# Kernel tuning notes

Measured on AMD Instinct MI355X. Metric: run time of the kernel, lower is better.

The kernel has to match this reference:

```python
import jax, jax.numpy as jnp
import numpy as np

N_SA_ITERS = 3
MESH_LR = 5.0
MESH_ITERS = 4
SH_ITERS = 5
EPS = 1e-8
B, N, D, S, H = 16, 16384, 64, 7, 128


def layer_norm(x, g, b):
    m = jnp.mean(x, -1, keepdims=True)
    v = jnp.var(x, -1, keepdims=True)
    return (x - m) * jax.lax.rsqrt(v + 1e-5) * g + b


def cdist(k, q):
    # k: [b,n,d], q: [b,s,d] -> euclidean distances [b,n,s]
    k2 = jnp.sum(k * k, -1)[:, :, None]
    q2 = jnp.sum(q * q, -1)[:, None, :]
    sq = k2 + q2 - 2.0 * jnp.einsum('bnd,bsd->bns', k, q)
    return jnp.sqrt(jnp.maximum(sq, 0.0) + 1e-12)


def sinkhorn(C, log_a, log_b, u, v, n_iters=SH_ITERS):
    # log-domain Sinkhorn. C: [b,n,s], log_a: [b,n], log_b: [b,s]
    p = -C
    for _ in range(n_iters):
        u = log_a - jax.nn.logsumexp(p + v[:, None, :], axis=2)
        v = log_b - jax.nn.logsumexp(p + u[:, :, None], axis=1)
    T = jnp.exp(p + u[:, :, None] + v[:, None, :])
    return T, u, v


def minimize_entropy_of_sinkhorn(C, log_a, log_b, mesh_lr=MESH_LR, n_mesh_iters=MESH_ITERS):
    # MESH: gradient descent on transport-plan entropy wrt the cost matrix,
    # warm-starting the sinkhorn duals across mesh iterations.
    u = jnp.zeros_like(log_a)
    v = jnp.zeros_like(log_b)
    for _ in range(n_mesh_iters):
        def ent(Cc, uu, vv):
            T, u2, v2 = sinkhorn(Cc, log_a, log_b, uu, vv)
            e = -jnp.sum(T * jnp.log(T + EPS))
            return e, (u2, v2)
        (_, (u, v)), g = jax.value_and_grad(ent, has_aux=True)(
            C, jax.lax.stop_gradient(u), jax.lax.stop_gradient(v))
        C = C - mesh_lr * g
    return C, u, v


def gru_cell(x, h, W_ih, W_hh, b_ih, b_hh):
    # PyTorch nn.GRUCell semantics
    gi = x @ W_ih.T + b_ih
    gh = h @ W_hh.T + b_hh
    i_r, i_z, i_n = jnp.split(gi, 3, axis=-1)
    h_r, h_z, h_n = jnp.split(gh, 3, axis=-1)
    r = jax.nn.sigmoid(i_r + h_r)
    z = jax.nn.sigmoid(i_z + h_z)
    n = jnp.tanh(i_n + r * h_n)
    return (1.0 - z) * n + z * h


def setup_inputs() -> dict:
    key = jax.random.key(0)
    ks = jax.random.split(key, 24)
    w = lambda k, shape, s=0.05: (jax.random.normal(k, shape, dtype=jnp.float32) * s)
    return {
        'inputs': jax.random.normal(ks[0], (B, N, D), dtype=jnp.float32),
        'slots_init': jax.random.normal(ks[1], (B, S, D), dtype=jnp.float32),
        'slots_mu': w(ks[2], (1, 1, D), 0.1),
        'slots_log_sigma': w(ks[3], (1, 1, D), 0.1),
        'Wq': w(ks[4], (D, D)), 'Wk': w(ks[5], (D, D)), 'Wv': w(ks[6], (D, D)),
        'gru_Wih': w(ks[7], (3 * D, D)), 'gru_Whh': w(ks[8], (3 * D, D)),
        'gru_bih': jnp.zeros((3 * D,), jnp.float32), 'gru_bhh': jnp.zeros((3 * D,), jnp.float32),
        'fc1_W': w(ks[9], (H, D)), 'fc1_b': jnp.zeros((H,), jnp.float32),
        'fc2_W': w(ks[10], (D, H)), 'fc2_b': jnp.zeros((D,), jnp.float32),
        'ln_in_g': jnp.ones((D,), jnp.float32), 'ln_in_b': jnp.zeros((D,), jnp.float32),
        'ln_sl_g': jnp.ones((D,), jnp.float32), 'ln_sl_b': jnp.zeros((D,), jnp.float32),
        'ln_ff_g': jnp.ones((D,), jnp.float32), 'ln_ff_b': jnp.zeros((D,), jnp.float32),
        'wi_W': w(ks[11], (1, D)), 'wi_b': jnp.zeros((1,), jnp.float32),
        'ws_W': w(ks[12], (1, D)), 'ws_b': jnp.zeros((1,), jnp.float32),
    }


def reference(inputs, slots_init, slots_mu, slots_log_sigma, Wq, Wk, Wv,
              gru_Wih, gru_Whh, gru_bih, gru_bhh, fc1_W, fc1_b, fc2_W, fc2_b,
              ln_in_g, ln_in_b, ln_sl_g, ln_sl_b, ln_ff_g, ln_ff_b,
              wi_W, wi_b, ws_W, ws_b):
    b_s, n_in, d = inputs.shape
    n_s = slots_init.shape[1]
    slots = slots_mu + jnp.exp(slots_log_sigma) * slots_init
    x = layer_norm(inputs, ln_in_g, ln_in_b)
    k = x @ Wk.T
    v = x @ Wv.T
    # input marginal a (sums to n_s over the n_in axis)
    a = jax.nn.softmax((x @ wi_W.T + wi_b)[..., 0], axis=-1) * n_s
    log_a = jnp.log(a)
    attn = None
    for _ in range(N_SA_ITERS):
        slots_prev = slots
        s_n = layer_norm(slots, ln_sl_g, ln_sl_b)
        b_marg = jax.nn.softmax((s_n @ ws_W.T + ws_b)[..., 0], axis=-1) * n_s
        log_b = jnp.log(b_marg)
        q = s_n @ Wq.T
        C = cdist(k, q)                                   # [b, n_in, n_s]
        C, p_u, q_v = minimize_entropy_of_sinkhorn(C, log_a, log_b)
        attn, _, _ = sinkhorn(C, log_a, log_b, p_u, q_v)  # [b, n_in, n_s]
        attn = jnp.transpose(attn, (0, 2, 1))             # [b, n_s, n_in]
        updates = jnp.matmul(attn, v)                     # [b, n_s, d]
        slots = gru_cell(updates.reshape(b_s * n_s, d), slots_prev.reshape(b_s * n_s, d),
                         gru_Wih, gru_Whh, gru_bih, gru_bhh).reshape(b_s, n_s, d)
        ff = jax.nn.relu(layer_norm(slots, ln_ff_g, ln_ff_b) @ fc1_W.T + fc1_b) @ fc2_W.T + fc2_b
        slots = slots + ff
    return slots, attn
```

## Files before the change

kernel.cpp:

```cpp
#include <hip/hip_runtime.h>
#include <math.h>

#define AGENTS __HIP_MEMORY_SCOPE_AGENT

constexpr int   CB   = 16;
constexpr int   CN   = 16384;
constexpr float LOG7 = 1.9459101090932196f;
constexpr float EPST = 1e-8f;

constexpr size_t OFF_PA  = 1088;
constexpr size_t OFF_RED = 1600;
constexpr size_t OFF_UPD = 5696;
constexpr size_t OFF_QSP = 120384;
constexpr size_t OFF_WQT = 513600;
constexpr size_t OFF_WIH = 517696;
constexpr size_t OFF_WHH = 529984;
constexpr size_t OFF_F1T = 542272;
constexpr size_t OFF_F2T = 550464;
constexpr size_t OFF_K   = 558656;
constexpr size_t OFF_V   = OFF_K + (size_t)CB * CN * 64;

__device__ __forceinline__ float aload(const float* p) {
  return __hip_atomic_load(const_cast<float*>(p), __ATOMIC_RELAXED, AGENTS);
}
__device__ __forceinline__ void astore(float* p, float v) {
  __hip_atomic_store(p, v, __ATOMIC_RELAXED, AGENTS);
}
__device__ __forceinline__ float wsum64(float v) {
#pragma unroll
  for (int m = 1; m < 64; m <<= 1) v += __shfl_xor(v, m, 64);
  return v;
}
__device__ __forceinline__ float dot4(float4 a, float4 b) {
  return a.x * b.x + a.y * b.y + a.z * b.z + a.w * b.w;
}

__device__ __forceinline__ void batch_sync(unsigned* cnt, unsigned& tgt) {
  asm volatile("s_waitcnt vmcnt(0)" ::: "memory");
  __syncthreads();
  tgt += 16;
  if (threadIdx.x == 0) {
    __hip_atomic_fetch_add(cnt, 1u, __ATOMIC_RELAXED, AGENTS);
    unsigned v;
    do {
      v = __hip_atomic_load(cnt, __ATOMIC_RELAXED, AGENTS);
      if (v < tgt) __builtin_amdgcn_s_sleep(1);
    } while (v < tgt);
  }
  __syncthreads();
}

__device__ __forceinline__ void reduce7_sync(float (&es)[7], float* __restrict__ wsp,
                                             float* s_redw, float* tot, int bb, int ib,
                                             unsigned* cnt, unsigned& tgt, int& rbuf) {
  const int tid = threadIdx.x, lane = tid & 63, wid = tid >> 6;
#pragma unroll
  for (int m = 1; m < 64; m <<= 1) {
#pragma unroll
    for (int s = 0; s < 7; ++s) es[s] += __shfl_xor(es[s], m, 64);
  }
  if (lane == 0) {
#pragma unroll
    for (int s = 0; s < 7; ++s) s_redw[wid * 8 + s] = es[s];
  }
  __syncthreads();
  float* rp = wsp + OFF_RED + (size_t)((rbuf * CB + bb) * 16) * 8;
  if (wid == 0) {
#pragma unroll
    for (int h = 0; h < 2; ++h) {
      int s = h * 4 + (lane >> 4);
      float v = 0.f;
      if (s < 7) v = s_redw[(lane & 15) * 8 + s];
      v += __shfl_xor(v, 1, 64); v += __shfl_xor(v, 2, 64);
      v += __shfl_xor(v, 4, 64); v += __shfl_xor(v, 8, 64);
      if ((lane & 15) == 0 && s < 7) astore(rp + ib * 8 + s, v);
    }
  }
  batch_sync(cnt, tgt);
  if (wid == 0) {
#pragma unroll
    for (int h = 0; h < 2; ++h) {
      int s = h * 4 + (lane >> 4);
      float v = 0.f;
      if (s < 7) v = aload(rp + (lane & 15) * 8 + s);
      v += __shfl_xor(v, 1, 64); v += __shfl_xor(v, 2, 64);
      v += __shfl_xor(v, 4, 64); v += __shfl_xor(v, 8, 64);
      if ((lane & 15) == 0 && s < 7) tot[s] = v;
    }
  }
  __syncthreads();
  rbuf ^= 1;
}

__global__ void prep_kernel(const float* __restrict__ Wq, const float* __restrict__ Wih,
                            const float* __restrict__ Whh, const float* __restrict__ f1,
                            const float* __restrict__ f2, float* __restrict__ w) {
  int idx = blockIdx.x * blockDim.x + threadIdx.x;
  int stride = gridDim.x * blockDim.x;
  if (idx < 1024) reinterpret_cast<unsigned*>(w)[idx] = 0u;
  for (int i = idx; i < 64 * 64; i += stride) {
    int d = i / 64, j = i % 64;
    w[OFF_WQT + j * 64 + d] = Wq[d * 64 + j];
  }
  for (int i = idx; i < 192 * 64; i += stride) {
    int o = i / 64, j = i % 64;
    w[OFF_WIH + j * 192 + o] = Wih[o * 64 + j];
    w[OFF_WHH + j * 192 + o] = Whh[o * 64 + j];
  }
  for (int i = idx; i < 128 * 64; i += stride) {
    int o = i / 64, j = i % 64;
    w[OFF_F1T + j * 128 + o] = f1[o * 64 + j];
  }
  for (int i = idx; i < 64 * 128; i += stride) {
    int d = i / 128, j = i % 128;
    w[OFF_F2T + j * 64 + d] = f2[d * 128 + j];
  }
}

__launch_bounds__(1024, 4)
__global__ void slot_attn_kernel(
    const float* __restrict__ inputs, const float* __restrict__ sinit,
    const float* __restrict__ smu, const float* __restrict__ slsig,
    const float* __restrict__ Wk, const float* __restrict__ Wv,
    const float* __restrict__ gbih, const float* __restrict__ gbhh,
    const float* __restrict__ fc1b, const float* __restrict__ fc2b,
    const float* __restrict__ lin_g, const float* __restrict__ lin_b,
    const float* __restrict__ lsl_g, const float* __restrict__ lsl_b,
    const float* __restrict__ lff_g, const float* __restrict__ lff_b,
    const float* __restrict__ wi_W, const float* __restrict__ wi_b,
    const float* __restrict__ wsW, const float* __restrict__ wsB,
    float* __restrict__ out, float* __restrict__ w) {
  __shared__ float s_slots[448];
  __shared__ float s_snl[448];
  __shared__ float s_scr1[1344];
  __shared__ float s_scr2[1344];
  __shared__ float s_updl[448];
  __shared__ float s_T[8192];
  __shared__ float s_pupd[7168];
  __shared__ float s_vh[48];
  __shared__ float s_logb[8];
  __shared__ float s_gvl[8];
  __shared__ float s_tot[8];
  __shared__ float s_wl[8];
  __shared__ float s_redw[128];
  __shared__ float s_misc[4];

  const int tid = threadIdx.x;
  const int lane = tid & 63, wid = tid >> 6;
  const int bb = blockIdx.x & 15;
  const int ib = blockIdx.x >> 4;
  const int nloc = ib * 1024 + tid;
  const size_t grow = (size_t)bb * CN + nloc;
  unsigned* cnt = reinterpret_cast<unsigned*>(w) + (size_t)bb * 64;
  unsigned tgt = 0;
  int rbuf = 0;
  float log_a;

  {
    const float* xin = inputs + grow * 64;
    float4 xa[16];
#pragma unroll
    for (int c = 0; c < 16; ++c) xa[c] = reinterpret_cast<const float4*>(xin)[c];
    float s1 = 0;
#pragma unroll
    for (int c = 0; c < 16; ++c) s1 += xa[c].x + xa[c].y + xa[c].z + xa[c].w;
    float mn = s1 * (1.f / 64.f);
    float s2 = 0;
#pragma unroll
    for (int c = 0; c < 16; ++c) {
      float dx = xa[c].x - mn, dy = xa[c].y - mn, dz = xa[c].z - mn, dw = xa[c].w - mn;
      s2 += dx * dx + dy * dy + dz * dz + dw * dw;
    }
    float rs = rsqrtf(s2 * (1.f / 64.f) + 1e-5f);
#pragma unroll
    for (int c = 0; c < 16; ++c) {
      float4 g4 = reinterpret_cast<const float4*>(lin_g)[c];
      float4 b4 = reinterpret_cast<const float4*>(lin_b)[c];
      xa[c].x = (xa[c].x - mn) * rs * g4.x + b4.x;
      xa[c].y = (xa[c].y - mn) * rs * g4.y + b4.y;
      xa[c].z = (xa[c].z - mn) * rs * g4.z + b4.z;
      xa[c].w = (xa[c].w - mn) * rs * g4.w + b4.w;
    }
    float lg = wi_b[0];
#pragma unroll
    for (int c = 0; c < 16; ++c) lg += dot4(xa[c], reinterpret_cast<const float4*>(wi_W)[c]);
#pragma unroll 1
    for (int half = 0; half < 2; ++half) {
      const float* W = half ? Wv : Wk;
      float* ob = w + (half ? OFF_V : OFF_K) + grow * 64;
#pragma unroll 1
      for (int oc = 0; oc < 8; ++oc) {
        float acc[8] = {0, 0, 0, 0, 0, 0, 0, 0};
#pragma unroll
        for (int c = 0; c < 16; ++c) {
          float4 xv = xa[c];
#pragma unroll
          for (int o8 = 0; o8 < 8; ++o8) {
            float4 w4 = reinterpret_cast<const float4*>(W + (size_t)(oc * 8 + o8) * 64)[c];
            acc[o8] += dot4(xv, w4);
          }
        }
        reinterpret_cast<float4*>(ob + oc * 8)[0] = make_float4(acc[0], acc[1], acc[2], acc[3]);
        reinterpret_cast<float4*>(ob + oc * 8)[1] = make_float4(acc[4], acc[5], acc[6], acc[7]);
      }
    }
    float mx = lg;
#pragma unroll
    for (int m = 1; m < 64; m <<= 1) mx = fmaxf(mx, __shfl_xor(mx, m, 64));
    float se = wsum64(__expf(lg - mx));
    if (lane == 0) { s_redw[wid * 8 + 0] = mx; s_redw[wid * 8 + 1] = se; }
    __syncthreads();
    float* pa = w + OFF_PA + (size_t)bb * 32;
    if (wid == 0 && lane < 16) {
      float m0 = s_redw[lane * 8 + 0], e0 = s_redw[lane * 8 + 1];
#pragma unroll
      for (int mm = 1; mm < 16; mm <<= 1) {
        float m1 = __shfl_xor(m0, mm, 64), e1 = __shfl_xor(e0, mm, 64);
        float nm = fmaxf(m0, m1);
        e0 = e0 * __expf(m0 - nm) + e1 * __expf(m1 - nm);
        m0 = nm;
      }
      if (lane == 0) { astore(pa + ib * 2 + 0, m0); astore(pa + ib * 2 + 1, e0); }
    }
    batch_sync(cnt, tgt);
    if (wid == 0 && lane < 16) {
      float m0 = aload(pa + lane * 2 + 0), e0 = aload(pa + lane * 2 + 1);
#pragma unroll
      for (int mm = 1; mm < 16; mm <<= 1) {
        float m1 = __shfl_xor(m0, mm, 64), e1 = __shfl_xor(e0, mm, 64);
        float nm = fmaxf(m0, m1);
        e0 = e0 * __expf(m0 - nm) + e1 * __expf(m1 - nm);
        m0 = nm;
      }
      if (lane == 0) s_misc[0] = m0 + __logf(e0);
    }
    __syncthreads();
    log_a = lg - s_misc[0] + LOG7;
  }

  auto slot_common = [&](int inst) {
    if (wid < 7) {
      float h = s_slots[wid * 64 + lane];
      float m = wsum64(h) * (1.f / 64.f);
      float d0 = h - m;
      float va = wsum64(d0 * d0) * (1.f / 64.f);
      float sn = d0 * rsqrtf(va + 1e-5f) * lsl_g[lane] + lsl_b[lane];
      s_snl[wid * 64 + lane] = sn;
      float pw = wsum64(sn * wsW[lane]);
      if (lane == 0) s_wl[wid] = pw + wsB[0];
    }
    __syncthreads();
    float* qsp = w + OFF_QSP + (size_t)(inst * 256 + blockIdx.x) * 512;
    if (tid < 448) {
      int s = tid >> 6, dd = tid & 63;
      float acc = 0;
#pragma unroll 4
      for (int j = 0; j < 64; ++j) acc += s_snl[s * 64 + j] * w[OFF_WQT + j * 64 + dd];
      qsp[s * 64 + dd] = acc;
      s_scr1[s * 64 + dd] = acc;
    }
    __syncthreads();
    if (wid < 7) {
      float qv = s_scr1[wid * 64 + lane];
      float q2 = wsum64(qv * qv);
      if (lane == 0) qsp[448 + wid] = q2;
    }
    if (tid == 0) {
      float mx = -1e30f;
#pragma unroll
      for (int s = 0; s < 7; ++s) mx = fmaxf(mx, s_wl[s]);
      float se = 0;
#pragma unroll
      for (int s = 0; s < 7; ++s) se += __expf(s_wl[s] - mx);
      float lse = mx + __logf(se);
#pragma unroll
      for (int s = 0; s < 7; ++s) s_logb[s] = s_wl[s] - lse + LOG7;
    }
    __syncthreads();
  };

  if (tid < 448) {
    int dd = tid & 63;
    s_slots[tid] = smu[dd] + __expf(slsig[dd]) * sinit[(size_t)bb * 448 + tid];
  }
  __syncthreads();
  slot_common(0);

  float p[7], u = 0.f;
  auto fwd5 = [&]() {
#pragma unroll 1
    for (int i = 1; i <= 5; ++i) {
      float t = 0;
#pragma unroll
      for (int s = 0; s < 7; ++s) t += __expf(p[s] + s_vh[(i - 1) * 8 + s]);
      u = log_a - __logf(t);
      float es[7];
#pragma unroll
      for (int s = 0; s < 7; ++s) es[s] = __expf(p[s] + u);
      reduce7_sync(es, w, s_redw, s_tot, bb, ib, cnt, tgt, rbuf);
      if (tid < 7) s_vh[i * 8 + tid] = s_logb[tid] - __logf(s_tot[tid]);
      __syncthreads();
    }
  };

#pragma unroll 1
  for (int it = 0; it < 3; ++it) {
    {
      const float* kb = w + OFF_K + grow * 64;
      const float* qsp = w + OFF_QSP + (size_t)(it * 256 + blockIdx.x) * 512;
      float k2 = 0, kq[7] = {0, 0, 0, 0, 0, 0, 0};
#pragma unroll
      for (int c = 0; c < 16; ++c) {
        float4 kk = reinterpret_cast<const float4*>(kb)[c];
        k2 += dot4(kk, kk);
#pragma unroll
        for (int s = 0; s < 7; ++s)
          kq[s] += dot4(kk, reinterpret_cast<const float4*>(qsp + s * 64)[c]);
      }
#pragma unroll
      for (int s = 0; s < 7; ++s) {
        float sq = k2 + qsp[448 + s] - 2.f * kq[s];
        p[s] = -sqrtf(fmaxf(sq, 0.f) + 1e-12f);
      }
    }
    if (tid < 8) s_vh[tid] = 0.f;
    __syncthreads();

#pragma unroll 1
    for (int ms = 0; ms < 4; ++ms) {
      fwd5();
      float gp[7], guT = 0.f;
      {
        float es[7];
#pragma unroll
        for (int s = 0; s < 7; ++s) {
          float T = __expf(p[s] + u + s_vh[40 + s]);
          float gT = -(__logf(T + EPST) + T / (T + EPST));
          float g = gT * T;
          gp[s] = g; guT += g; es[s] = g;
        }
        reduce7_sync(es, w, s_redw, s_gvl, bb, ib, cnt, tgt, rbuf);
      }
#pragma unroll 1
      for (int i = 5; i >= 1; --i) {
        float t = 0;
#pragma unroll
        for (int s = 0; s < 7; ++s) t += __expf(p[s] + s_vh[(i - 1) * 8 + s]);
        float ui = log_a - __logf(t);
        float gu = (i == 5) ? guT : 0.f;
#pragma unroll
        for (int s = 0; s < 7; ++s) {
          float sn = __expf(p[s] + ui - s_logb[s] + s_vh[i * 8 + s]);
          float gz = -s_gvl[s] * sn;
          gp[s] += gz; gu += gz;
        }
        float gw[7];
#pragma unroll
        for (int s = 0; s < 7; ++s) {
          float sg = __expf(p[s] + s_vh[(i - 1) * 8 + s] - log_a + ui);
          gw[s] = -gu * sg;
          gp[s] += gw[s];
        }
        if (i > 1) reduce7_sync(gw, w, s_redw, s_gvl, bb, ib, cnt, tgt, rbuf);
      }
#pragma unroll
      for (int s = 0; s < 7; ++s) p[s] -= 5.0f * gp[s];
      if (tid < 8) s_vh[tid] = s_vh[40 + tid];
      __syncthreads();
    }

    fwd5();
    float T7[7];
#pragma unroll
    for (int s = 0; s < 7; ++s) T7[s] = __expf(p[s] + u + s_vh[40 + s]);
    if (it == 2) {
      size_t ab = 7168 + (size_t)(bb * 7) * CN + nloc;
#pragma unroll
      for (int s = 0; s < 7; ++s) out[ab + (size_t)s * CN] = T7[s];
    }
#pragma unroll
    for (int s = 0; s < 7; ++s) s_T[tid * 8 + s] = T7[s];
    s_T[tid * 8 + 7] = 0.f;
    __syncthreads();

    {
      const float* vb = w + OFF_V + (size_t)(bb * CN + ib * 1024 + wid * 64) * 64 + lane;
      float acc[7] = {0, 0, 0, 0, 0, 0, 0};
#pragma unroll 4
      for (int n = 0; n < 64; ++n) {
        float vv = vb[(size_t)n * 64];
        const float* tr = &s_T[(wid * 64 + n) * 8];
        acc[0] += tr[0] * vv; acc[1] += tr[1] * vv; acc[2] += tr[2] * vv;
        acc[3] += tr[3] * vv; acc[4] += tr[4] * vv; acc[5] += tr[5] * vv;
        acc[6] += tr[6] * vv;
      }
#pragma unroll
      for (int s = 0; s < 7; ++s) s_pupd[(wid * 7 + s) * 64 + lane] = acc[s];
    }
    __syncthreads();
    if (tid < 448) {
      int s = tid >> 6, dd = tid & 63;
      float t = 0;
#pragma unroll
      for (int w16 = 0; w16 < 16; ++w16) t += s_pupd[(w16 * 7 + s) * 64 + dd];
      astore(w + OFF_UPD + (size_t)((bb * 16 + ib) * 7 + s) * 64 + dd, t);
    }
    batch_sync(cnt, tgt);
    if (tid < 448) {
      int s = tid >> 6, dd = tid & 63;
      float t = 0;
#pragma unroll
      for (int j = 0; j < 16; ++j)
        t += aload(w + OFF_UPD + (size_t)((bb * 16 + j) * 7 + s) * 64 + dd);
      s_updl[s * 64 + dd] = t;
    }
    __syncthreads();

    {
#pragma unroll 1
      for (int idx = tid; idx < 1344; idx += 1024) {
        int s = idx / 192, o = idx - s * 192;
        float g1 = gbih[o], g2 = gbhh[o];
#pragma unroll 4
        for (int j = 0; j < 64; ++j) {
          g1 += s_updl[s * 64 + j] * w[OFF_WIH + j * 192 + o];
          g2 += s_slots[s * 64 + j] * w[OFF_WHH + j * 192 + o];
        }
        s_scr1[s * 192 + o] = g1;
        s_scr2[s * 192 + o] = g2;
      }
      __syncthreads();
      if (tid < 448) {
        int s = tid >> 6, dd = tid & 63;
        float ir = s_scr1[s * 192 + dd],       hr = s_scr2[s * 192 + dd];
        float iz = s_scr1[s * 192 + 64 + dd],  hz = s_scr2[s * 192 + 64 + dd];
        float in_ = s_scr1[s * 192 + 128 + dd], hn = s_scr2[s * 192 + 128 + dd];
        float r = 1.f / (1.f + __expf(-(ir + hr)));
        float z = 1.f / (1.f + __expf(-(iz + hz)));
        float nn = tanhf(in_ + r * hn);
        s_updl[s * 64 + dd] = (1.f - z) * nn + z * s_slots[s * 64 + dd];
      }
      __syncthreads();
      if (wid < 7) {
        float h = s_updl[wid * 64 + lane];
        float m = wsum64(h) * (1.f / 64.f);
        float d0 = h - m;
        float va = wsum64(d0 * d0) * (1.f / 64.f);
        s_snl[wid * 64 + lane] = d0 * rsqrtf(va + 1e-5f) * lff_g[lane] + lff_b[lane];
      }
      __syncthreads();
      if (tid < 896) {
        int s = tid >> 7, i2 = tid & 127;
        float a1 = fc1b[i2];
#pragma unroll 4
        for (int j = 0; j < 64; ++j) a1 += s_snl[s * 64 + j] * w[OFF_F1T + j * 128 + i2];
        s_scr1[s * 128 + i2] = fmaxf(a1, 0.f);
      }
      __syncthreads();
      if (tid < 448) {
        int s = tid >> 6, dd = tid & 63;
        float a2 = fc2b[dd];
#pragma unroll 4
        for (int i2 = 0; i2 < 128; ++i2) a2 += s_scr1[s * 128 + i2] * w[OFF_F2T + i2 * 64 + dd];
        s_slots[s * 64 + dd] = s_updl[s * 64 + dd] + a2;
      }
      __syncthreads();
    }
    if (it < 2) slot_common(it + 1);
  }

  if (ib == 0 && tid < 448) out[(size_t)bb * 448 + tid] = s_slots[tid];
}

extern "C" void kernel_launch(void* const* d_in, const int* in_sizes, int n_in,
                              void* d_out, int out_size, void* d_ws, size_t ws_size,
                              hipStream_t stream) {
  (void)in_sizes; (void)n_in; (void)out_size; (void)ws_size;
  const float* inputs = (const float*)d_in[0];
  const float* sinit  = (const float*)d_in[1];
  const float* smu    = (const float*)d_in[2];
  const float* slsig  = (const float*)d_in[3];
  const float* Wq     = (const float*)d_in[4];
  const float* Wk     = (const float*)d_in[5];
  const float* Wv     = (const float*)d_in[6];
  const float* gWih   = (const float*)d_in[7];
  const float* gWhh   = (const float*)d_in[8];
  const float* gbih   = (const float*)d_in[9];
  const float* gbhh   = (const float*)d_in[10];
  const float* fc1W   = (const float*)d_in[11];
  const float* fc1b   = (const float*)d_in[12];
  const float* fc2W   = (const float*)d_in[13];
  const float* fc2b   = (const float*)d_in[14];
  const float* ling   = (const float*)d_in[15];
  const float* linb   = (const float*)d_in[16];
  const float* lslg   = (const float*)d_in[17];
  const float* lslb   = (const float*)d_in[18];
  const float* lffg   = (const float*)d_in[19];
  const float* lffb   = (const float*)d_in[20];
  const float* wiW    = (const float*)d_in[21];
  const float* wib    = (const float*)d_in[22];
  const float* wsW    = (const float*)d_in[23];
  const float* wsb    = (const float*)d_in[24];
  float* out = (float*)d_out;
  float* w   = (float*)d_ws;

  prep_kernel<<<dim3(64), dim3(256), 0, stream>>>(Wq, gWih, gWhh, fc1W, fc2W, w);
  slot_attn_kernel<<<dim3(256), dim3(1024), 0, stream>>>(
      inputs, sinit, smu, slsig, Wk, Wv, gbih, gbhh, fc1b, fc2b,
      ling, linb, lslg, lslb, lffg, lffb, wiW, wib, wsW, wsb, out, w);
}
```

Measured before the change: 2.007 ms.

## Consolidate per-batch work into 4 blocks with epoch-tagged flag exchanges

After the input projection phase, only one in four blocks per batch continues; each surviving block handles four row chunks held in registers, so the Sinkhorn/MESH reductions exchange partials among 4 blocks instead of 16. The counter-based barrier is replaced by 64-bit value+epoch packed stores that readers poll directly, removing the separate barrier round trip. The q projection stays in shared memory instead of going through global scratch. In exchange, each remaining block does four times the per-row work serially and holds more register state, which may reduce occupancy, and most of the GPU idles during the iterative phase.

```diff
diff --git a/kernel.cpp b/kernel.cpp
--- a/kernel.cpp
+++ b/kernel.cpp
@@ -2,29 +2,39 @@
 #include <math.h>
 
 #define AGENTS __HIP_MEMORY_SCOPE_AGENT
+typedef unsigned long long u64x;
 
 constexpr int   CB   = 16;
 constexpr int   CN   = 16384;
 constexpr float LOG7 = 1.9459101090932196f;
 constexpr float EPST = 1e-8f;
 
-constexpr size_t OFF_PA  = 1088;
-constexpr size_t OFF_RED = 1600;
-constexpr size_t OFF_UPD = 5696;
-constexpr size_t OFF_QSP = 120384;
-constexpr size_t OFF_WQT = 513600;
-constexpr size_t OFF_WIH = 517696;
-constexpr size_t OFF_WHH = 529984;
-constexpr size_t OFF_F1T = 542272;
-constexpr size_t OFF_F2T = 550464;
-constexpr size_t OFF_K   = 558656;
+constexpr size_t ST1 = 0;
+constexpr size_t ST2 = 512;
+constexpr size_t ST3 = 1536;
+constexpr size_t NST = 58880;
+
+constexpr size_t OFF_LG  = 117760;
+constexpr size_t OFF_WQT = 379904;
+constexpr size_t OFF_WIH = 384000;
+constexpr size_t OFF_WHH = 396288;
+constexpr size_t OFF_F1T = 408576;
+constexpr size_t OFF_F2T = 416768;
+constexpr size_t OFF_K   = 424960;
 constexpr size_t OFF_V   = OFF_K + (size_t)CB * CN * 64;
 
-__device__ __forceinline__ float aload(const float* p) {
-  return __hip_atomic_load(const_cast<float*>(p), __ATOMIC_RELAXED, AGENTS);
-}
-__device__ __forceinline__ void astore(float* p, float v) {
+__device__ __forceinline__ u64x pk(float v, unsigned e) {
+  return ((u64x)e << 32) | (u64x)__float_as_uint(v);
+}
+__device__ __forceinline__ void st_rlx(u64x* p, u64x v) {
   __hip_atomic_store(p, v, __ATOMIC_RELAXED, AGENTS);
+}
+__device__ __forceinline__ float poll_val(const u64x* p, unsigned e) {
+  u64x q;
+  do {
+    q = __hip_atomic_load(const_cast<u64x*>(p), __ATOMIC_RELAXED, AGENTS);
+  } while ((unsigned)(q >> 32) != e);
+  return __uint_as_float((unsigned)q);
 }
 __device__ __forceinline__ float wsum64(float v) {
 #pragma unroll
@@ -33,63 +43,6 @@
 }
 __device__ __forceinline__ float dot4(float4 a, float4 b) {
   return a.x * b.x + a.y * b.y + a.z * b.z + a.w * b.w;
-}
-
-__device__ __forceinline__ void batch_sync(unsigned* cnt, unsigned& tgt) {
-  asm volatile("s_waitcnt vmcnt(0)" ::: "memory");
-  __syncthreads();
-  tgt += 16;
-  if (threadIdx.x == 0) {
-    __hip_atomic_fetch_add(cnt, 1u, __ATOMIC_RELAXED, AGENTS);
-    unsigned v;
-    do {
-      v = __hip_atomic_load(cnt, __ATOMIC_RELAXED, AGENTS);
-      if (v < tgt) __builtin_amdgcn_s_sleep(1);
-    } while (v < tgt);
-  }
-  __syncthreads();
-}
-
-__device__ __forceinline__ void reduce7_sync(float (&es)[7], float* __restrict__ wsp,
-                                             float* s_redw, float* tot, int bb, int ib,
-                                             unsigned* cnt, unsigned& tgt, int& rbuf) {
-  const int tid = threadIdx.x, lane = tid & 63, wid = tid >> 6;
-#pragma unroll
-  for (int m = 1; m < 64; m <<= 1) {
-#pragma unroll
-    for (int s = 0; s < 7; ++s) es[s] += __shfl_xor(es[s], m, 64);
-  }
-  if (lane == 0) {
-#pragma unroll
-    for (int s = 0; s < 7; ++s) s_redw[wid * 8 + s] = es[s];
-  }
-  __syncthreads();
-  float* rp = wsp + OFF_RED + (size_t)((rbuf * CB + bb) * 16) * 8;
-  if (wid == 0) {
-#pragma unroll
-    for (int h = 0; h < 2; ++h) {
-      int s = h * 4 + (lane >> 4);
-      float v = 0.f;
-      if (s < 7) v = s_redw[(lane & 15) * 8 + s];
-      v += __shfl_xor(v, 1, 64); v += __shfl_xor(v, 2, 64);
-      v += __shfl_xor(v, 4, 64); v += __shfl_xor(v, 8, 64);
-      if ((lane & 15) == 0 && s < 7) astore(rp + ib * 8 + s, v);
-    }
-  }
-  batch_sync(cnt, tgt);
-  if (wid == 0) {
-#pragma unroll
-    for (int h = 0; h < 2; ++h) {
-      int s = h * 4 + (lane >> 4);
-      float v = 0.f;
-      if (s < 7) v = aload(rp + (lane & 15) * 8 + s);
-      v += __shfl_xor(v, 1, 64); v += __shfl_xor(v, 2, 64);
-      v += __shfl_xor(v, 4, 64); v += __shfl_xor(v, 8, 64);
-      if ((lane & 15) == 0 && s < 7) tot[s] = v;
-    }
-  }
-  __syncthreads();
-  rbuf ^= 1;
 }
 
 __global__ void prep_kernel(const float* __restrict__ Wq, const float* __restrict__ Wih,
@@ -97,7 +50,8 @@
                             const float* __restrict__ f2, float* __restrict__ w) {
   int idx = blockIdx.x * blockDim.x + threadIdx.x;
   int stride = gridDim.x * blockDim.x;
-  if (idx < 1024) reinterpret_cast<unsigned*>(w)[idx] = 0u;
+  u64x* st = reinterpret_cast<u64x*>(w);
+  for (size_t i = idx; i < NST; i += stride) st_rlx(st + i, 0ULL);
   for (int i = idx; i < 64 * 64; i += stride) {
     int d = i / 64, j = i % 64;
     w[OFF_WQT + j * 64 + d] = Wq[d * 64 + j];
@@ -132,6 +86,7 @@
     float* __restrict__ out, float* __restrict__ w) {
   __shared__ float s_slots[448];
   __shared__ float s_snl[448];
+  __shared__ float s_q[448];
   __shared__ float s_scr1[1344];
   __shared__ float s_scr2[1344];
   __shared__ float s_updl[448];
@@ -140,23 +95,21 @@
   __shared__ float s_vh[48];
   __shared__ float s_logb[8];
   __shared__ float s_gvl[8];
-  __shared__ float s_tot[8];
+  __shared__ float s_q2[8];
   __shared__ float s_wl[8];
   __shared__ float s_redw[128];
+  __shared__ float s_part[32];
   __shared__ float s_misc[4];
 
   const int tid = threadIdx.x;
   const int lane = tid & 63, wid = tid >> 6;
   const int bb = blockIdx.x & 15;
   const int ib = blockIdx.x >> 4;
-  const int nloc = ib * 1024 + tid;
-  const size_t grow = (size_t)bb * CN + nloc;
-  unsigned* cnt = reinterpret_cast<unsigned*>(w) + (size_t)bb * 64;
-  unsigned tgt = 0;
-  int rbuf = 0;
-  float log_a;
+  u64x* st = reinterpret_cast<u64x*>(w);
+  float lg;
 
   {
+    const size_t grow = (size_t)bb * CN + ib * 1024 + tid;
     const float* xin = inputs + grow * 64;
     float4 xa[16];
 #pragma unroll
@@ -181,9 +134,10 @@
       xa[c].z = (xa[c].z - mn) * rs * g4.z + b4.z;
       xa[c].w = (xa[c].w - mn) * rs * g4.w + b4.w;
     }
-    float lg = wi_b[0];
+    lg = wi_b[0];
 #pragma unroll
     for (int c = 0; c < 16; ++c) lg += dot4(xa[c], reinterpret_cast<const float4*>(wi_W)[c]);
+    w[OFF_LG + grow] = lg;
 #pragma unroll 1
     for (int half = 0; half < 2; ++half) {
       const float* W = half ? Wv : Wk;
@@ -209,10 +163,11 @@
     for (int m = 1; m < 64; m <<= 1) mx = fmaxf(mx, __shfl_xor(mx, m, 64));
     float se = wsum64(__expf(lg - mx));
     if (lane == 0) { s_redw[wid * 8 + 0] = mx; s_redw[wid * 8 + 1] = se; }
-    __syncthreads();
-    float* pa = w + OFF_PA + (size_t)bb * 32;
-    if (wid == 0 && lane < 16) {
-      float m0 = s_redw[lane * 8 + 0], e0 = s_redw[lane * 8 + 1];
+    asm volatile("s_waitcnt vmcnt(0)" ::: "memory");
+    __syncthreads();
+    if (wid == 0) {
+      float m0 = (lane < 16) ? s_redw[lane * 8 + 0] : -1e30f;
+      float e0 = (lane < 16) ? s_redw[lane * 8 + 1] : 0.f;
 #pragma unroll
       for (int mm = 1; mm < 16; mm <<= 1) {
         float m1 = __shfl_xor(m0, mm, 64), e1 = __shfl_xor(e0, mm, 64);
@@ -220,25 +175,109 @@
         e0 = e0 * __expf(m0 - nm) + e1 * __expf(m1 - nm);
         m0 = nm;
       }
-      if (lane == 0) { astore(pa + ib * 2 + 0, m0); astore(pa + ib * 2 + 1, e0); }
-    }
-    batch_sync(cnt, tgt);
-    if (wid == 0 && lane < 16) {
-      float m0 = aload(pa + lane * 2 + 0), e0 = aload(pa + lane * 2 + 1);
-#pragma unroll
-      for (int mm = 1; mm < 16; mm <<= 1) {
-        float m1 = __shfl_xor(m0, mm, 64), e1 = __shfl_xor(e0, mm, 64);
-        float nm = fmaxf(m0, m1);
-        e0 = e0 * __expf(m0 - nm) + e1 * __expf(m1 - nm);
-        m0 = nm;
-      }
-      if (lane == 0) s_misc[0] = m0 + __logf(e0);
-    }
-    __syncthreads();
-    log_a = lg - s_misc[0] + LOG7;
-  }
-
-  auto slot_common = [&](int inst) {
+      __threadfence();
+      if (lane == 0) {
+        st_rlx(st + ST1 + ((size_t)bb * 16 + ib) * 2 + 0, pk(m0, 1u));
+        st_rlx(st + ST1 + ((size_t)bb * 16 + ib) * 2 + 1, pk(e0, 1u));
+      }
+    }
+  }
+
+  if (ib & 3) return;
+  const int sc = ib >> 2;
+
+  if (wid == 0) {
+    float m0 = -1e30f, e0 = 0.f;
+    if (lane < 16) {
+      m0 = poll_val(st + ST1 + ((size_t)bb * 16 + lane) * 2 + 0, 1u);
+      e0 = poll_val(st + ST1 + ((size_t)bb * 16 + lane) * 2 + 1, 1u);
+    }
+#pragma unroll
+    for (int mm = 1; mm < 16; mm <<= 1) {
+      float m1 = __shfl_xor(m0, mm, 64), e1 = __shfl_xor(e0, mm, 64);
+      float nm = fmaxf(m0, m1);
+      e0 = e0 * __expf(m0 - nm) + e1 * __expf(m1 - nm);
+      m0 = nm;
+    }
+    __threadfence();
+    if (lane == 0) s_misc[0] = m0 + __logf(e0);
+  }
+  __syncthreads();
+  float log_a[4];
+  {
+    float lse = s_misc[0];
+    log_a[0] = lg - lse + LOG7;
+#pragma unroll
+    for (int r = 1; r < 4; ++r) {
+      float lgr = w[OFF_LG + (size_t)bb * CN + sc * 4096 + r * 1024 + tid];
+      log_a[r] = lgr - lse + LOG7;
+    }
+  }
+
+  unsigned e = 2;
+  float p[4][7], u[4];
+
+  auto exchange4 = [&](float (&es)[7], float* dst8, bool to_vh) {
+#pragma unroll
+    for (int m = 1; m < 64; m <<= 1) {
+#pragma unroll
+      for (int s = 0; s < 7; ++s) es[s] += __shfl_xor(es[s], m, 64);
+    }
+    if (lane < 7) s_redw[wid * 8 + lane] = es[lane];
+    __syncthreads();
+    const unsigned par = e & 1;
+    u64x* sl2 = st + ST2 + ((size_t)(bb * 2 + par) * 4) * 8;
+    if (wid == 0) {
+      float bp[2]; int ss[2];
+#pragma unroll
+      for (int h = 0; h < 2; ++h) {
+        int s = h * 4 + (lane >> 4); ss[h] = s;
+        float v = (s < 7) ? s_redw[(lane & 15) * 8 + s] : 0.f;
+        v += __shfl_xor(v, 1, 64); v += __shfl_xor(v, 2, 64);
+        v += __shfl_xor(v, 4, 64); v += __shfl_xor(v, 8, 64);
+        bp[h] = v;
+      }
+      if ((lane & 15) == 0) {
+#pragma unroll
+        for (int h = 0; h < 2; ++h) {
+          if (ss[h] < 7) {
+            st_rlx(sl2 + sc * 8 + ss[h], pk(bp[h], e));
+            s_part[24 + ss[h]] = bp[h];
+          }
+        }
+      }
+      int rj = lane >> 3, s = lane & 7;
+      if (rj < 3 && s < 7) {
+        int rsc = rj + (rj >= sc);
+        s_part[rj * 8 + s] = poll_val(sl2 + rsc * 8 + s, e);
+      }
+      if (lane < 7) {
+        float tot = s_part[lane] + s_part[8 + lane] + s_part[16 + lane] + s_part[24 + lane];
+        dst8[lane] = to_vh ? (s_logb[lane] - __logf(tot)) : tot;
+      }
+    }
+    __syncthreads();
+    ++e;
+  };
+
+  auto fwd5 = [&]() {
+#pragma unroll 1
+    for (int i = 1; i <= 5; ++i) {
+      float es[7] = {0, 0, 0, 0, 0, 0, 0};
+#pragma unroll
+      for (int r = 0; r < 4; ++r) {
+        float t = 0;
+#pragma unroll
+        for (int s = 0; s < 7; ++s) t += __expf(p[r][s] + s_vh[(i - 1) * 8 + s]);
+        u[r] = log_a[r] - __logf(t);
+#pragma unroll
+        for (int s = 0; s < 7; ++s) es[s] += __expf(p[r][s] + u[r]);
+      }
+      exchange4(es, s_vh + i * 8, true);
+    }
+  };
+
+  auto slot_common = [&]() {
     if (wid < 7) {
       float h = s_slots[wid * 64 + lane];
       float m = wsum64(h) * (1.f / 64.f);
@@ -250,20 +289,18 @@
       if (lane == 0) s_wl[wid] = pw + wsB[0];
     }
     __syncthreads();
-    float* qsp = w + OFF_QSP + (size_t)(inst * 256 + blockIdx.x) * 512;
     if (tid < 448) {
       int s = tid >> 6, dd = tid & 63;
       float acc = 0;
 #pragma unroll 4
       for (int j = 0; j < 64; ++j) acc += s_snl[s * 64 + j] * w[OFF_WQT + j * 64 + dd];
-      qsp[s * 64 + dd] = acc;
-      s_scr1[s * 64 + dd] = acc;
+      s_q[s * 64 + dd] = acc;
     }
     __syncthreads();
     if (wid < 7) {
-      float qv = s_scr1[wid * 64 + lane];
+      float qv = s_q[wid * 64 + lane];
       float q2 = wsum64(qv * qv);
-      if (lane == 0) qsp[448 + wid] = q2;
+      if (lane == 0) s_q2[wid] = q2;
     }
     if (tid == 0) {
       float mx = -1e30f;
@@ -284,43 +321,27 @@
     s_slots[tid] = smu[dd] + __expf(slsig[dd]) * sinit[(size_t)bb * 448 + tid];
   }
   __syncthreads();
-  slot_common(0);
-
-  float p[7], u = 0.f;
-  auto fwd5 = [&]() {
-#pragma unroll 1
-    for (int i = 1; i <= 5; ++i) {
-      float t = 0;
-#pragma unroll
-      for (int s = 0; s < 7; ++s) t += __expf(p[s] + s_vh[(i - 1) * 8 + s]);
-      u = log_a - __logf(t);
-      float es[7];
-#pragma unroll
-      for (int s = 0; s < 7; ++s) es[s] = __expf(p[s] + u);
-      reduce7_sync(es, w, s_redw, s_tot, bb, ib, cnt, tgt, rbuf);
-      if (tid < 7) s_vh[i * 8 + tid] = s_logb[tid] - __logf(s_tot[tid]);
-      __syncthreads();
-    }
-  };
+  slot_common();
 
 #pragma unroll 1
   for (int it = 0; it < 3; ++it) {
-    {
-      const float* kb = w + OFF_K + grow * 64;
-      const float* qsp = w + OFF_QSP + (size_t)(it * 256 + blockIdx.x) * 512;
-      float k2 = 0, kq[7] = {0, 0, 0, 0, 0, 0, 0};
-#pragma unroll
-      for (int c = 0; c < 16; ++c) {
-        float4 kk = reinterpret_cast<const float4*>(kb)[c];
-        k2 += dot4(kk, kk);
-#pragma unroll
-        for (int s = 0; s < 7; ++s)
-          kq[s] += dot4(kk, reinterpret_cast<const float4*>(qsp + s * 64)[c]);
-      }
+#pragma unroll 1
+    for (int r = 0; r < 4; ++r) {
+      const float* kb = w + OFF_K + ((size_t)bb * CN + sc * 4096 + r * 1024 + tid) * 64;
+      float4 ka[16];
+#pragma unroll
+      for (int c = 0; c < 16; ++c) ka[c] = reinterpret_cast<const float4*>(kb)[c];
+      float k2 = 0;
+#pragma unroll
+      for (int c = 0; c < 16; ++c) k2 += dot4(ka[c], ka[c]);
 #pragma unroll
       for (int s = 0; s < 7; ++s) {
-        float sq = k2 + qsp[448 + s] - 2.f * kq[s];
-        p[s] = -sqrtf(fmaxf(sq, 0.f) + 1e-12f);
+        float kq = 0;
+#pragma unroll
+        for (int c = 0; c < 16; ++c)
+          kq += dot4(ka[c], *reinterpret_cast<const float4*>(&s_q[s * 64 + c * 4]));
+        float sq = k2 + s_q2[s] - 2.f * kq;
+        p[r][s] = -sqrtf(fmaxf(sq, 0.f) + 1e-12f);
       }
     }
     if (tid < 8) s_vh[tid] = 0.f;
@@ -329,63 +350,73 @@
 #pragma unroll 1
     for (int ms = 0; ms < 4; ++ms) {
       fwd5();
-      float gp[7], guT = 0.f;
+      float gp[4][7], gu0[4];
       {
-        float es[7];
-#pragma unroll
-        for (int s = 0; s < 7; ++s) {
-          float T = __expf(p[s] + u + s_vh[40 + s]);
-          float gT = -(__logf(T + EPST) + T / (T + EPST));
-          float g = gT * T;
-          gp[s] = g; guT += g; es[s] = g;
+        float es[7] = {0, 0, 0, 0, 0, 0, 0};
+#pragma unroll
+        for (int r = 0; r < 4; ++r) {
+          gu0[r] = 0.f;
+#pragma unroll
+          for (int s = 0; s < 7; ++s) {
+            float T = __expf(p[r][s] + u[r] + s_vh[40 + s]);
+            float gT = -(__logf(T + EPST) + T / (T + EPST));
+            float g = gT * T;
+            gp[r][s] = g; gu0[r] += g; es[s] += g;
+          }
         }
-        reduce7_sync(es, w, s_redw, s_gvl, bb, ib, cnt, tgt, rbuf);
+        exchange4(es, s_gvl, false);
       }
 #pragma unroll 1
       for (int i = 5; i >= 1; --i) {
-        float t = 0;
-#pragma unroll
-        for (int s = 0; s < 7; ++s) t += __expf(p[s] + s_vh[(i - 1) * 8 + s]);
-        float ui = log_a - __logf(t);
-        float gu = (i == 5) ? guT : 0.f;
-#pragma unroll
-        for (int s = 0; s < 7; ++s) {
-          float sn = __expf(p[s] + ui - s_logb[s] + s_vh[i * 8 + s]);
-          float gz = -s_gvl[s] * sn;
-          gp[s] += gz; gu += gz;
+        float es[7] = {0, 0, 0, 0, 0, 0, 0};
+#pragma unroll
+        for (int r = 0; r < 4; ++r) {
+          float t = 0;
+#pragma unroll
+          for (int s = 0; s < 7; ++s) t += __expf(p[r][s] + s_vh[(i - 1) * 8 + s]);
+          float ui = log_a[r] - __logf(t);
+          float gu = (i == 5) ? gu0[r] : 0.f;
+#pragma unroll
+          for (int s = 0; s < 7; ++s) {
+            float sn = __expf(p[r][s] + ui - s_logb[s] + s_vh[i * 8 + s]);
+            float gz = -s_gvl[s] * sn;
+            gp[r][s] += gz; gu += gz;
+          }
+#pragma unroll
+          for (int s = 0; s < 7; ++s) {
+            float sg = __expf(p[r][s] + s_vh[(i - 1) * 8 + s] - log_a[r] + ui);
+            float gw = -gu * sg;
+            gp[r][s] += gw; es[s] += gw;
+          }
         }
-        float gw[7];
-#pragma unroll
-        for (int s = 0; s < 7; ++s) {
-          float sg = __expf(p[s] + s_vh[(i - 1) * 8 + s] - log_a + ui);
-          gw[s] = -gu * sg;
-          gp[s] += gw[s];
-        }
-        if (i > 1) reduce7_sync(gw, w, s_redw, s_gvl, bb, ib, cnt, tgt, rbuf);
-      }
-#pragma unroll
-      for (int s = 0; s < 7; ++s) p[s] -= 5.0f * gp[s];
+        if (i > 1) exchange4(es, s_gvl, false);
+      }
+#pragma unroll
+      for (int r = 0; r < 4; ++r)
+#pragma unroll
+        for (int s = 0; s < 7; ++s) p[r][s] -= 5.0f * gp[r][s];
       if (tid < 8) s_vh[tid] = s_vh[40 + tid];
       __syncthreads();
     }
 
     fwd5();
-    float T7[7];
-#pragma unroll
-    for (int s = 0; s < 7; ++s) T7[s] = __expf(p[s] + u + s_vh[40 + s]);
-    if (it == 2) {
-      size_t ab = 7168 + (size_t)(bb * 7) * CN + nloc;
-#pragma unroll
-      for (int s = 0; s < 7; ++s) out[ab + (size_t)s * CN] = T7[s];
-    }
-#pragma unroll
-    for (int s = 0; s < 7; ++s) s_T[tid * 8 + s] = T7[s];
-    s_T[tid * 8 + 7] = 0.f;
-    __syncthreads();
-
-    {
-      const float* vb = w + OFF_V + (size_t)(bb * CN + ib * 1024 + wid * 64) * 64 + lane;
-      float acc[7] = {0, 0, 0, 0, 0, 0, 0};
+    float acc[7] = {0, 0, 0, 0, 0, 0, 0};
+#pragma unroll 1
+    for (int r = 0; r < 4; ++r) {
+      float tv[7];
+#pragma unroll
+      for (int s = 0; s < 7; ++s) tv[s] = __expf(p[r][s] + u[r] + s_vh[40 + s]);
+      if (it == 2) {
+        size_t rowg = (size_t)sc * 4096 + r * 1024 + tid;
+#pragma unroll
+        for (int s = 0; s < 7; ++s)
+          out[7168 + ((size_t)(bb * 7 + s)) * CN + rowg] = tv[s];
+      }
+#pragma unroll
+      for (int s = 0; s < 7; ++s) s_T[tid * 8 + s] = tv[s];
+      __syncthreads();
+      const float* vb = w + OFF_V +
+          ((size_t)bb * CN + sc * 4096 + r * 1024 + wid * 64) * 64 + lane;
 #pragma unroll 4
       for (int n = 0; n < 64; ++n) {
         float vv = vb[(size_t)n * 64];
@@ -394,27 +425,28 @@
         acc[3] += tr[3] * vv; acc[4] += tr[4] * vv; acc[5] += tr[5] * vv;
         acc[6] += tr[6] * vv;
       }
-#pragma unroll
-      for (int s = 0; s < 7; ++s) s_pupd[(wid * 7 + s) * 64 + lane] = acc[s];
-    }
-    __syncthreads();
-    if (tid < 448) {
-      int s = tid >> 6, dd = tid & 63;
-      float t = 0;
-#pragma unroll
-      for (int w16 = 0; w16 < 16; ++w16) t += s_pupd[(w16 * 7 + s) * 64 + dd];
-      astore(w + OFF_UPD + (size_t)((bb * 16 + ib) * 7 + s) * 64 + dd, t);
-    }
-    batch_sync(cnt, tgt);
-    if (tid < 448) {
-      int s = tid >> 6, dd = tid & 63;
-      float t = 0;
-#pragma unroll
-      for (int j = 0; j < 16; ++j)
-        t += aload(w + OFF_UPD + (size_t)((bb * 16 + j) * 7 + s) * 64 + dd);
-      s_updl[s * 64 + dd] = t;
-    }
-    __syncthreads();
+      __syncthreads();
+    }
+#pragma unroll
+    for (int s = 0; s < 7; ++s) s_pupd[(wid * 7 + s) * 64 + lane] = acc[s];
+    __syncthreads();
+    {
+      const unsigned par = e & 1;
+      u64x* sl3 = st + ST3 + ((size_t)(bb * 2 + par) * 4) * 448;
+      if (tid < 448) {
+        float t = 0;
+#pragma unroll
+        for (int w16 = 0; w16 < 16; ++w16) t += s_pupd[w16 * 448 + tid];
+        st_rlx(sl3 + sc * 448 + tid, pk(t, e));
+        float tot = 0;
+#pragma unroll 1
+        for (int j = 0; j < 4; ++j)
+          tot += (j == sc) ? t : poll_val(sl3 + (size_t)j * 448 + tid, e);
+        s_updl[tid] = tot;
+      }
+      __syncthreads();
+      ++e;
+    }
 
     {
 #pragma unroll 1
@@ -432,8 +464,8 @@
       __syncthreads();
       if (tid < 448) {
         int s = tid >> 6, dd = tid & 63;
-        float ir = s_scr1[s * 192 + dd],       hr = s_scr2[s * 192 + dd];
-        float iz = s_scr1[s * 192 + 64 + dd],  hz = s_scr2[s * 192 + 64 + dd];
+        float ir = s_scr1[s * 192 + dd],        hr = s_scr2[s * 192 + dd];
+        float iz = s_scr1[s * 192 + 64 + dd],   hz = s_scr2[s * 192 + 64 + dd];
         float in_ = s_scr1[s * 192 + 128 + dd], hn = s_scr2[s * 192 + 128 + dd];
         float r = 1.f / (1.f + __expf(-(ir + hr)));
         float z = 1.f / (1.f + __expf(-(iz + hz)));
@@ -466,10 +498,10 @@
       }
       __syncthreads();
     }
-    if (it < 2) slot_common(it + 1);
-  }
-
-  if (ib == 0 && tid < 448) out[(size_t)bb * 448 + tid] = s_slots[tid];
+    if (it < 2) slot_common();
+  }
+
+  if (sc == 0 && tid < 448) out[(size_t)bb * 448 + tid] = s_slots[tid];
 }
 
 extern "C" void kernel_launch(void* const* d_in, const int* in_sizes, int n_in,
```

New measurement: 3.304 ms. +64.6%, slower.
